# Kernel optimization log

Measured on AMD Instinct MI355X. Metric: run time of the kernel, lower is better.

## Reference

```python
import jax, jax.numpy as jnp
import numpy as np

TAU = 2.0
VTH = 0.7
VRESET = 0.0
ALPHA = 4.0
MAX_ITER = 10
WARM = 2
T, B, F = 1024, 32, 512


def setup_inputs() -> dict:
    key = jax.random.key(0)
    x = jax.random.normal(key, (T, B, F), dtype=jnp.float32)
    v_init = jnp.zeros((B, F), dtype=jnp.float32)
    return {"x": x, "v_init": v_init}


def _shift(y, y_init):
    # [y_init, y[0], ..., y[T-2]]
    return jnp.concatenate([y_init[None], y[:-1]], axis=0)


def _solve_linear_recurrence(a, b, y0):
    # y[t] = a[t] * y[t-1] + b[t], y[-1] = y0; parallel via associative scan
    def comb(l, r):
        al, bl = l
        ar, br = r
        return ar * al, ar * bl + br
    A, Bc = jax.lax.associative_scan(comb, (a, b))
    return A * y0[None] + Bc


def _warmstart(x, v_init):
    # first K steps of the continuous (no-reset) dynamics, rest zeros
    K = min(WARM, x.shape[0])
    v = v_init
    rows = []
    for t in range(K):  # K=2, tiny fixed unroll
        h = v + (x[t] - v) / TAU
        rows.append(h)
        v = h
    guess = jnp.zeros_like(x)
    return guess.at[:K].set(jnp.stack(rows, axis=0))


def _forward(x, v_init):
    y = _warmstart(x, v_init)
    decay = 1.0 - 1.0 / TAU
    for _ in range(MAX_ITER):  # fixed iteration count (check_convergence=False)
        ys = _shift(y, v_init)            # (T,B,F)
        h = ys + (x - ys) / TAU           # L[y]: continuous dynamics, no reset
        hc = jnp.clip(h, -20.0, 20.0)
        s = jax.nn.sigmoid(ALPHA * (hc - VTH))
        sg = ALPHA * s * (1.0 - s)        # surrogate gradient
        G = -(decay * (1.0 - sg * (1.0 - VRESET)))  # diagonal Jacobian (T,B,F)
        rhs = h + G * ys
        y = _solve_linear_recurrence(-G, rhs, v_init)
    spike = (y >= VTH).astype(y.dtype)
    return spike, y


def reference(x, v_init):
    return _forward(x, v_init)
```

## Files before the change

kernel.cpp:

```cpp
#include <hip/hip_runtime.h>

#pragma clang fp contract(off)

namespace {
constexpr int B_ = 32;
constexpr int F_ = 512;
constexpr int BF_ = B_ * F_;
constexpr long TBF_ = 16777216;
constexpr int NITER = 10;
constexpr int NTHR = 256;

typedef float v2f __attribute__((ext_vector_type(2)));

constexpr float KLOG = 5.770780163555852f;
constexpr float CLOG = 4.0395461144890964f;

__device__ __forceinline__ int swz(int bb) { return bb ^ ((bb >> 3) & 7); }

struct ABp { v2f A, B; };
__device__ __forceinline__ ABp combp(ABp l, ABp r) {
  ABp o;
  o.A = r.A * l.A;
  o.B = __builtin_elementwise_fma(r.A, l.B, r.B);
  return o;
}

template <int CTRL, int RM>
__device__ __forceinline__ float dppf(float oldv, float src) {
  return __builtin_bit_cast(
      float, __builtin_amdgcn_update_dpp(__builtin_bit_cast(int, oldv),
                                         __builtin_bit_cast(int, src), CTRL,
                                         RM, 0xf, false));
}

template <int CTRL, int RM>
__device__ __forceinline__ ABp scan_step(ABp S) {
  ABp P;
  P.A.x = dppf<CTRL, RM>(1.0f, S.A.x);
  P.A.y = dppf<CTRL, RM>(1.0f, S.A.y);
  P.B.x = dppf<CTRL, RM>(0.0f, S.B.x);
  P.B.y = dppf<CTRL, RM>(0.0f, S.B.y);
  return combp(P, S);
}

__device__ __forceinline__ v2f pkfma(v2f a, v2f b, v2f c) {
  return __builtin_elementwise_fma(a, b, c);
}
}

__global__ __launch_bounds__(NTHR, 4) void deer_lif_kernel(
    const float* __restrict__ x, const float* __restrict__ v_init,
    float* __restrict__ out) {
  __shared__ float smem[8192];

  const int raw = blockIdx.x;
  const int blk = (raw & 7) * 256 + (raw >> 3);

  const int b  = blk >> 6;
  const int f0 = (blk & 63) << 3;

  const int tid = threadIdx.x;
  const int rt = tid >> 1;
  const int c0 = (tid & 1) << 2;
  const int wr0 = c0 >> 1;

  const float* xb = x + (long)b * F_ + f0 + c0;
#pragma unroll
  for (int p = 0; p < 8; ++p) {
    const int t = rt + (p << 7);
    const float4 v = *reinterpret_cast<const float4*>(xb + (long)t * BF_);
    const int base = (swz(t >> 1) << 2) + ((t & 1) << 1);
    *reinterpret_cast<float2*>(&smem[wr0 * 2048 + base]) =
        make_float2(v.x, v.y);
    *reinterpret_cast<float2*>(&smem[(wr0 + 1) * 2048 + base]) =
        make_float2(v.z, v.w);
  }
  __syncthreads();

  const int w = tid >> 6;
  const int lane = tid & 63;
  const bool lz = (lane == 0);
  const float* colb = &smem[w * 2048];

  const float2 vi =
      *reinterpret_cast<const float2*>(&v_init[b * F_ + f0 + 2 * w]);
  v2f v0 = {vi.x, vi.y};

  v2f y[16];
#pragma unroll
  for (int j = 0; j < 16; ++j) y[j] = (v2f){0.0f, 0.0f};
  if (lz) {
    const float4 v = *reinterpret_cast<const float4*>(&colb[0]);
    const v2f x0 = {v.x, v.y};
    const v2f x1 = {v.z, v.w};
    const v2f h0 = v0 + (x0 - v0) * 0.5f;
    const v2f h1 = h0 + (x1 - h0) * 0.5f;
    y[0] = h0;
    y[1] = h1;
  }

  const v2f half2 = {0.5f, 0.5f};
  const v2f one2 = {1.0f, 1.0f};
  const v2f nk2 = {-KLOG, -KLOG};
  const v2f ck2 = {CLOG, CLOG};
  const v2f lo2 = {-20.0f, -20.0f};
  const v2f m22 = {-2.0f, -2.0f};

#pragma unroll 1
  for (int it = 0; it < NITER; ++it) {
    v2f ys0;
    ys0.x = dppf<0x138, 0xf>(v0.x, y[15].x);
    ys0.y = dppf<0x138, 0xf>(v0.y, y[15].y);

    v2f a[16], r[16];
#pragma unroll
    for (int q = 0; q < 8; ++q) {
      const int bbs = swz((lane << 3) + q);
      const float4 xv = *reinterpret_cast<const float4*>(&colb[bbs << 2]);
#pragma unroll
      for (int u = 0; u < 2; ++u) {
        const int j = 2 * q + u;
        const v2f xj = u ? (v2f){xv.z, xv.w} : (v2f){xv.x, xv.y};
        const v2f ys = (j == 0) ? ys0 : y[j - 1];
        const v2f d = xj - ys;
        const v2f h = pkfma(d, half2, ys);
        const v2f hc = __builtin_elementwise_max(h, lo2);
        const v2f z = pkfma(hc, nk2, ck2);
        v2f e;
        e.x = __builtin_amdgcn_exp2f(z.x);
        e.y = __builtin_amdgcn_exp2f(z.y);
        const v2f den = one2 + e;
        v2f s;
        s.x = __builtin_amdgcn_rcpf(den.x);
        s.y = __builtin_amdgcn_rcpf(den.y);
        const v2f oms = one2 - s;
        const v2f pp = s * oms;
        const v2f aj = pkfma(pp, m22, half2);
        const v2f rj = pkfma(-aj, ys, h);
        a[j] = aj;
        r[j] = rj;
      }
    }

    v2f qA0 = a[0], qB0 = r[0];
    v2f qA1 = a[4], qB1 = r[4];
    v2f qA2 = a[8], qB2 = r[8];
    v2f qA3 = a[12], qB3 = r[12];
#pragma unroll
    for (int k = 1; k < 4; ++k) {
      qA0 = qA0 * a[k];      qB0 = pkfma(qB0, a[k], r[k]);
      qA1 = qA1 * a[4 + k];  qB1 = pkfma(qB1, a[4 + k], r[4 + k]);
      qA2 = qA2 * a[8 + k];  qB2 = pkfma(qB2, a[8 + k], r[8 + k]);
      qA3 = qA3 * a[12 + k]; qB3 = pkfma(qB3, a[12 + k], r[12 + k]);
    }
    const v2f c01A = qA0 * qA1, c01B = pkfma(qB0, qA1, qB1);
    const v2f c012A = c01A * qA2, c012B = pkfma(c01B, qA2, qB2);
    ABp S;
    S.A = c012A * qA3;
    S.B = pkfma(c012B, qA3, qB3);

    S = scan_step<0x111, 0xf>(S);
    S = scan_step<0x112, 0xf>(S);
    S = scan_step<0x114, 0xf>(S);
    S = scan_step<0x118, 0xf>(S);
    S = scan_step<0x142, 0xa>(S);
    S = scan_step<0x143, 0xc>(S);

    const v2f cinc = pkfma(S.A, v0, S.B);
    v2f cin;
    cin.x = dppf<0x138, 0xf>(v0.x, cinc.x);
    cin.y = dppf<0x138, 0xf>(v0.y, cinc.y);

    v2f t0 = cin;
    v2f t1 = pkfma(qA0, cin, qB0);
    v2f t2 = pkfma(c01A, cin, c01B);
    v2f t3 = pkfma(c012A, cin, c012B);
#pragma unroll
    for (int k = 0; k < 4; ++k) {
      t0 = pkfma(a[k], t0, r[k]);           y[k] = t0;
      t1 = pkfma(a[4 + k], t1, r[4 + k]);   y[4 + k] = t1;
      t2 = pkfma(a[8 + k], t2, r[8 + k]);   y[8 + k] = t2;
      t3 = pkfma(a[12 + k], t3, r[12 + k]); y[12 + k] = t3;
    }
  }

#pragma unroll
  for (int q = 0; q < 8; ++q) {
    const int bbs = swz((lane << 3) + q);
    float4 v;
    v.x = y[2 * q].x;
    v.y = y[2 * q].y;
    v.z = y[2 * q + 1].x;
    v.w = y[2 * q + 1].y;
    *reinterpret_cast<float4*>(&smem[w * 2048 + (bbs << 2)]) = v;
  }
  __syncthreads();

  float* outs = out;
  float* outy = out + TBF_;
  const long cb = (long)b * F_ + f0 + c0;
#pragma unroll
  for (int p = 0; p < 8; ++p) {
    const int t = rt + (p << 7);
    const int base = (swz(t >> 1) << 2) + ((t & 1) << 1);
    const float2 lo = *reinterpret_cast<const float2*>(&smem[wr0 * 2048 + base]);
    const float2 h2 =
        *reinterpret_cast<const float2*>(&smem[(wr0 + 1) * 2048 + base]);
    const float4 yv = make_float4(lo.x, lo.y, h2.x, h2.y);
    const float4 sv = make_float4(yv.x >= 0.7f ? 1.0f : 0.0f,
                                  yv.y >= 0.7f ? 1.0f : 0.0f,
                                  yv.z >= 0.7f ? 1.0f : 0.0f,
                                  yv.w >= 0.7f ? 1.0f : 0.0f);
    const long off = (long)t * BF_ + cb;
    *reinterpret_cast<float4*>(outy + off) = yv;
    *reinterpret_cast<float4*>(outs + off) = sv;
  }
}

extern "C" void kernel_launch(void* const* d_in, const int* in_sizes, int n_in,
                              void* d_out, int out_size, void* d_ws, size_t ws_size,
                              hipStream_t stream) {
  const float* x = (const float*)d_in[0];
  const float* v_init = (const float*)d_in[1];
  float* out = (float*)d_out;
  deer_lif_kernel<<<dim3(2048), dim3(NTHR), 0, stream>>>(x, v_init, out);
}
```

Before: 77.13 us.

## Use one wave per feature column with 512 threads instead of two

Each block now runs 8 waves instead of 4, one per feature, where before each wave handled two features packed as float2. Each lane now processes 16 consecutive timesteps of a single feature. Packed math is applied across adjacent timesteps, and the chunk combine uses a pairwise tree. This doubles the threads working on the serial recurrence and halves per-thread register state, aiming for more latency hiding. In exchange it adds scalar DPP scan work per feature and does strided 4-byte LDS reads that may cause bank conflicts.

```diff
diff --git a/kernel.cpp b/kernel.cpp
--- a/kernel.cpp
+++ b/kernel.cpp
@@ -8,7 +8,7 @@
 constexpr int BF_ = B_ * F_;
 constexpr long TBF_ = 16777216;
 constexpr int NITER = 10;
-constexpr int NTHR = 256;
+constexpr int NTHR = 512;
 
 typedef float v2f __attribute__((ext_vector_type(2)));
 
@@ -16,14 +16,6 @@
 constexpr float CLOG = 4.0395461144890964f;
 
 __device__ __forceinline__ int swz(int bb) { return bb ^ ((bb >> 3) & 7); }
-
-struct ABp { v2f A, B; };
-__device__ __forceinline__ ABp combp(ABp l, ABp r) {
-  ABp o;
-  o.A = r.A * l.A;
-  o.B = __builtin_elementwise_fma(r.A, l.B, r.B);
-  return o;
-}
 
 template <int CTRL, int RM>
 __device__ __forceinline__ float dppf(float oldv, float src) {
@@ -33,14 +25,16 @@
                                          RM, 0xf, false));
 }
 
+struct ABs { float A, B; };
 template <int CTRL, int RM>
-__device__ __forceinline__ ABp scan_step(ABp S) {
-  ABp P;
-  P.A.x = dppf<CTRL, RM>(1.0f, S.A.x);
-  P.A.y = dppf<CTRL, RM>(1.0f, S.A.y);
-  P.B.x = dppf<CTRL, RM>(0.0f, S.B.x);
-  P.B.y = dppf<CTRL, RM>(0.0f, S.B.y);
-  return combp(P, S);
+__device__ __forceinline__ ABs scan_step(ABs S) {
+  ABs P;
+  P.A = dppf<CTRL, RM>(1.0f, S.A);
+  P.B = dppf<CTRL, RM>(0.0f, S.B);
+  ABs o;
+  o.A = S.A * P.A;
+  o.B = __builtin_fmaf(S.A, P.B, S.B);
+  return o;
 }
 
 __device__ __forceinline__ v2f pkfma(v2f a, v2f b, v2f c) {
@@ -66,8 +60,8 @@
 
   const float* xb = x + (long)b * F_ + f0 + c0;
 #pragma unroll
-  for (int p = 0; p < 8; ++p) {
-    const int t = rt + (p << 7);
+  for (int p = 0; p < 4; ++p) {
+    const int t = rt + (p << 8);
     const float4 v = *reinterpret_cast<const float4*>(xb + (long)t * BF_);
     const int base = (swz(t >> 1) << 2) + ((t & 1) << 1);
     *reinterpret_cast<float2*>(&smem[wr0 * 2048 + base]) =
@@ -80,23 +74,22 @@
   const int w = tid >> 6;
   const int lane = tid & 63;
   const bool lz = (lane == 0);
-  const float* colb = &smem[w * 2048];
-
-  const float2 vi =
-      *reinterpret_cast<const float2*>(&v_init[b * F_ + f0 + 2 * w]);
-  v2f v0 = {vi.x, vi.y};
-
-  v2f y[16];
-#pragma unroll
-  for (int j = 0; j < 16; ++j) y[j] = (v2f){0.0f, 0.0f};
+  float* cb = &smem[(w >> 1) * 2048 + (w & 1)];
+
+  int fo[8];
+#pragma unroll
+  for (int p = 0; p < 8; ++p) fo[p] = swz((lane << 3) + p) << 2;
+
+  const float v0 = v_init[b * F_ + f0 + w];
+
+  v2f y2[8];
+#pragma unroll
+  for (int p = 0; p < 8; ++p) y2[p] = (v2f){0.0f, 0.0f};
   if (lz) {
-    const float4 v = *reinterpret_cast<const float4*>(&colb[0]);
-    const v2f x0 = {v.x, v.y};
-    const v2f x1 = {v.z, v.w};
-    const v2f h0 = v0 + (x0 - v0) * 0.5f;
-    const v2f h1 = h0 + (x1 - h0) * 0.5f;
-    y[0] = h0;
-    y[1] = h1;
+    const float x0 = cb[0], x1 = cb[2];
+    const float h0 = v0 + (x0 - v0) * 0.5f;
+    const float h1 = h0 + (x1 - h0) * 0.5f;
+    y2[0] = (v2f){h0, h1};
   }
 
   const v2f half2 = {0.5f, 0.5f};
@@ -108,56 +101,55 @@
 
 #pragma unroll 1
   for (int it = 0; it < NITER; ++it) {
-    v2f ys0;
-    ys0.x = dppf<0x138, 0xf>(v0.x, y[15].x);
-    ys0.y = dppf<0x138, 0xf>(v0.y, y[15].y);
-
-    v2f a[16], r[16];
-#pragma unroll
-    for (int q = 0; q < 8; ++q) {
-      const int bbs = swz((lane << 3) + q);
-      const float4 xv = *reinterpret_cast<const float4*>(&colb[bbs << 2]);
-#pragma unroll
-      for (int u = 0; u < 2; ++u) {
-        const int j = 2 * q + u;
-        const v2f xj = u ? (v2f){xv.z, xv.w} : (v2f){xv.x, xv.y};
-        const v2f ys = (j == 0) ? ys0 : y[j - 1];
-        const v2f d = xj - ys;
-        const v2f h = pkfma(d, half2, ys);
-        const v2f hc = __builtin_elementwise_max(h, lo2);
-        const v2f z = pkfma(hc, nk2, ck2);
-        v2f e;
-        e.x = __builtin_amdgcn_exp2f(z.x);
-        e.y = __builtin_amdgcn_exp2f(z.y);
-        const v2f den = one2 + e;
-        v2f s;
-        s.x = __builtin_amdgcn_rcpf(den.x);
-        s.y = __builtin_amdgcn_rcpf(den.y);
-        const v2f oms = one2 - s;
-        const v2f pp = s * oms;
-        const v2f aj = pkfma(pp, m22, half2);
-        const v2f rj = pkfma(-aj, ys, h);
-        a[j] = aj;
-        r[j] = rj;
-      }
-    }
-
-    v2f qA0 = a[0], qB0 = r[0];
-    v2f qA1 = a[4], qB1 = r[4];
-    v2f qA2 = a[8], qB2 = r[8];
-    v2f qA3 = a[12], qB3 = r[12];
-#pragma unroll
-    for (int k = 1; k < 4; ++k) {
-      qA0 = qA0 * a[k];      qB0 = pkfma(qB0, a[k], r[k]);
-      qA1 = qA1 * a[4 + k];  qB1 = pkfma(qB1, a[4 + k], r[4 + k]);
-      qA2 = qA2 * a[8 + k];  qB2 = pkfma(qB2, a[8 + k], r[8 + k]);
-      qA3 = qA3 * a[12 + k]; qB3 = pkfma(qB3, a[12 + k], r[12 + k]);
-    }
-    const v2f c01A = qA0 * qA1, c01B = pkfma(qB0, qA1, qB1);
-    const v2f c012A = c01A * qA2, c012B = pkfma(c01B, qA2, qB2);
-    ABp S;
-    S.A = c012A * qA3;
-    S.B = pkfma(c012B, qA3, qB3);
+    const float ys0 = dppf<0x138, 0xf>(v0, y2[7].y);
+
+    v2f a2[8], r2[8];
+#pragma unroll
+    for (int p = 0; p < 8; ++p) {
+      v2f xj;
+      xj.x = cb[fo[p]];
+      xj.y = cb[fo[p] + 2];
+      v2f ys;
+      ys.x = (p == 0) ? ys0 : y2[p - 1].y;
+      ys.y = y2[p].x;
+      const v2f d = xj - ys;
+      const v2f h = pkfma(d, half2, ys);
+      const v2f hc = __builtin_elementwise_max(h, lo2);
+      const v2f z = pkfma(hc, nk2, ck2);
+      v2f e;
+      e.x = __builtin_amdgcn_exp2f(z.x);
+      e.y = __builtin_amdgcn_exp2f(z.y);
+      const v2f den = one2 + e;
+      v2f s;
+      s.x = __builtin_amdgcn_rcpf(den.x);
+      s.y = __builtin_amdgcn_rcpf(den.y);
+      const v2f oms = one2 - s;
+      const v2f pp = s * oms;
+      const v2f aj = pkfma(pp, m22, half2);
+      const v2f rj = pkfma(-aj, ys, h);
+      a2[p] = aj;
+      r2[p] = rj;
+    }
+
+    float pA[8], pB[8];
+#pragma unroll
+    for (int p = 0; p < 8; ++p) {
+      pA[p] = a2[p].y * a2[p].x;
+      pB[p] = __builtin_fmaf(a2[p].y, r2[p].x, r2[p].y);
+    }
+    float qA[4], qB[4];
+#pragma unroll
+    for (int i = 0; i < 4; ++i) {
+      qA[i] = pA[2 * i + 1] * pA[2 * i];
+      qB[i] = __builtin_fmaf(pA[2 * i + 1], pB[2 * i], pB[2 * i + 1]);
+    }
+    const float c01A = qA[1] * qA[0];
+    const float c01B = __builtin_fmaf(qA[1], qB[0], qB[1]);
+    const float c012A = qA[2] * c01A;
+    const float c012B = __builtin_fmaf(qA[2], c01B, qB[2]);
+    ABs S;
+    S.A = qA[3] * c012A;
+    S.B = __builtin_fmaf(qA[3], c012B, qB[3]);
 
     S = scan_step<0x111, 0xf>(S);
     S = scan_step<0x112, 0xf>(S);
@@ -166,42 +158,41 @@
     S = scan_step<0x142, 0xa>(S);
     S = scan_step<0x143, 0xc>(S);
 
-    const v2f cinc = pkfma(S.A, v0, S.B);
-    v2f cin;
-    cin.x = dppf<0x138, 0xf>(v0.x, cinc.x);
-    cin.y = dppf<0x138, 0xf>(v0.y, cinc.y);
-
-    v2f t0 = cin;
-    v2f t1 = pkfma(qA0, cin, qB0);
-    v2f t2 = pkfma(c01A, cin, c01B);
-    v2f t3 = pkfma(c012A, cin, c012B);
-#pragma unroll
-    for (int k = 0; k < 4; ++k) {
-      t0 = pkfma(a[k], t0, r[k]);           y[k] = t0;
-      t1 = pkfma(a[4 + k], t1, r[4 + k]);   y[4 + k] = t1;
-      t2 = pkfma(a[8 + k], t2, r[8 + k]);   y[8 + k] = t2;
-      t3 = pkfma(a[12 + k], t3, r[12 + k]); y[12 + k] = t3;
-    }
-  }
-
-#pragma unroll
-  for (int q = 0; q < 8; ++q) {
-    const int bbs = swz((lane << 3) + q);
-    float4 v;
-    v.x = y[2 * q].x;
-    v.y = y[2 * q].y;
-    v.z = y[2 * q + 1].x;
-    v.w = y[2 * q + 1].y;
-    *reinterpret_cast<float4*>(&smem[w * 2048 + (bbs << 2)]) = v;
+    const float cinc = __builtin_fmaf(S.A, v0, S.B);
+    const float cin = dppf<0x138, 0xf>(v0, cinc);
+
+    const float s1 = __builtin_fmaf(qA[0], cin, qB[0]);
+    const float s2 = __builtin_fmaf(c01A, cin, c01B);
+    const float s3 = __builtin_fmaf(c012A, cin, c012B);
+#pragma unroll
+    for (int i = 0; i < 4; ++i) {
+      const float si = (i == 0) ? cin : (i == 1) ? s1 : (i == 2) ? s2 : s3;
+      v2f m1, b1;
+      m1.x = a2[2 * i].x;  m1.y = pA[2 * i];
+      b1.x = r2[2 * i].x;  b1.y = pB[2 * i];
+      const v2f w1 = pkfma(m1, (v2f){si, si}, b1);
+      y2[2 * i] = w1;
+      v2f m2, b2;
+      m2.x = a2[2 * i + 1].x;  m2.y = pA[2 * i + 1];
+      b2.x = r2[2 * i + 1].x;  b2.y = pB[2 * i + 1];
+      const v2f w2 = pkfma(m2, (v2f){w1.y, w1.y}, b2);
+      y2[2 * i + 1] = w2;
+    }
+  }
+
+#pragma unroll
+  for (int p = 0; p < 8; ++p) {
+    cb[fo[p]] = y2[p].x;
+    cb[fo[p] + 2] = y2[p].y;
   }
   __syncthreads();
 
   float* outs = out;
   float* outy = out + TBF_;
-  const long cb = (long)b * F_ + f0 + c0;
-#pragma unroll
-  for (int p = 0; p < 8; ++p) {
-    const int t = rt + (p << 7);
+  const long cbg = (long)b * F_ + f0 + c0;
+#pragma unroll
+  for (int p = 0; p < 4; ++p) {
+    const int t = rt + (p << 8);
     const int base = (swz(t >> 1) << 2) + ((t & 1) << 1);
     const float2 lo = *reinterpret_cast<const float2*>(&smem[wr0 * 2048 + base]);
     const float2 h2 =
@@ -211,7 +202,7 @@
                                   yv.y >= 0.7f ? 1.0f : 0.0f,
                                   yv.z >= 0.7f ? 1.0f : 0.0f,
                                   yv.w >= 0.7f ? 1.0f : 0.0f);
-    const long off = (long)t * BF_ + cb;
+    const long off = (long)t * BF_ + cbg;
     *reinterpret_cast<float4*>(outy + off) = yv;
     *reinterpret_cast<float4*>(outs + off) = sv;
   }
```

Measured after the change: 84.52 us. 9.6% more time.
